# Optimization experiments

Measured on AMD Instinct MI355X. Metric: run time of the kernel, lower is better.

## Reference

```python
import math
import jax, jax.numpy as jnp
import numpy as np

# Gemma4Audio config constants
HID = 1024
H = 8
D = HID // H            # 128
CHUNK = 12              # attention_chunk_size
PAST = 13 - 1           # max_past_horizon = context_left - 1
FUT = 0                 # max_future_horizon = context_right
CTX = CHUNK + PAST + FUT  # 24
SOFTCAP = 50.0
Q_SCALE = D ** (-0.5) / math.log(2)
K_SCALE = math.log(1.0 + math.e) / math.log(2)


def setup_inputs() -> dict:
    key = jax.random.key(0)
    ks = jax.random.split(key, 8)
    B, S = 4, 6144
    P = CTX + 1  # 25 relative positions
    std = HID ** (-0.5)
    return {
        "hidden_states": jax.random.normal(ks[0], (B, S, HID), jnp.float32),
        "position_embeddings": jax.random.normal(ks[1], (P, HID), jnp.float32),
        "Wq": jax.random.normal(ks[2], (HID, HID), jnp.float32) * std,
        "Wk": jax.random.normal(ks[3], (HID, HID), jnp.float32) * std,
        "Wv": jax.random.normal(ks[4], (HID, HID), jnp.float32) * std,
        "Wpost": jax.random.normal(ks[5], (HID, HID), jnp.float32) * std,
        "Wrel": jax.random.normal(ks[6], (HID, HID), jnp.float32) * std,
        "per_dim_scale": jnp.zeros((D,), jnp.float32),  # torch init: zeros
    }


def _extract_block_context(x, num_blocks):
    # x: [B, S, H, D] -> [B, num_blocks, CTX, H, D]
    xp = jnp.pad(x, ((0, 0), (PAST, FUT + CHUNK - 1), (0, 0), (0, 0)))
    idx = jnp.arange(num_blocks)[:, None] * CHUNK + jnp.arange(CTX)[None, :]
    return xp[:, idx]  # gather along seq axis


def _rel_shift(x):
    # x: [B, H, nb, CHUNK, P] -> [B, H, nb, CHUNK, CTX]
    B, Hh, nb, bs, pos_len = x.shape
    x = jnp.pad(x, ((0, 0), (0, 0), (0, 0), (0, 0), (0, CTX + 1 - pos_len)))
    x = x.reshape(B, Hh, nb, bs * (CTX + 1))[..., : bs * CTX]
    return x.reshape(B, Hh, nb, bs, CTX)


def reference(hidden_states, position_embeddings, Wq, Wk, Wv, Wpost, Wrel, per_dim_scale):
    B, S, _ = hidden_states.shape
    nb = (S + CHUNK - 1) // CHUNK
    pad = nb * CHUNK - S

    # Projections (ClippableLinear clamps are +/-inf at init -> identity)
    q = (hidden_states @ Wq.T).reshape(B, S, H, D)
    k = (hidden_states @ Wk.T).reshape(B, S, H, D)
    v = (hidden_states @ Wv.T).reshape(B, S, H, D)

    q = q * (Q_SCALE * jax.nn.softplus(per_dim_scale))  # per-dim scaled queries
    k = k * K_SCALE

    # [B, nb, CHUNK, H, D]
    q_blocked = jnp.pad(q, ((0, 0), (0, pad), (0, 0), (0, 0))).reshape(B, nb, CHUNK, H, D)
    k_ctx = _extract_block_context(k, nb)  # [B, nb, CTX, H, D]
    v_ctx = _extract_block_context(v, nb)

    # content score: [B, H, nb, CHUNK, CTX]
    matrix_ac = jnp.einsum('bnchd,bnkhd->bhnck', q_blocked, k_ctx)

    # relative position score
    rel_k = (position_embeddings @ Wrel.T).reshape(-1, H, D)  # [P, H, D]
    matrix_bd = jnp.einsum('bnchd,phd->bhncp', q_blocked, rel_k)
    matrix_bd = _rel_shift(matrix_bd)  # [B, H, nb, CHUNK, CTX]

    logits = matrix_ac + matrix_bd
    logits = jnp.tanh(logits / SOFTCAP) * SOFTCAP  # softcap
    attn = jax.nn.softmax(logits, axis=-1)

    out = jnp.einsum('bhnck,bnkhd->bnchd', attn, v_ctx)
    out = out.reshape(B, nb * CHUNK, H * D)[:, :S]
    return out @ Wpost.T
```

## Files before the change

### kernel.cpp

```cpp
#include <hip/hip_runtime.h>
#include <hip/hip_bf16.h>
#include <math.h>

typedef unsigned short ushort_t;
typedef __attribute__((ext_vector_type(8))) short short8;
typedef __attribute__((ext_vector_type(4))) short s4v;
typedef __attribute__((ext_vector_type(4))) float float4v;

#define HID 1024
#define NH 8
#define DH 128
#define CHUNK 12
#define PAST 12
#define CTX 24
#define NPOS 25
#define QKVW 3072

__device__ __forceinline__ float bf2f(ushort_t b){
  union{unsigned int u; float f;} x; x.u = ((unsigned int)b)<<16; return x.f;
}
__device__ __forceinline__ ushort_t f2bf(float f){
  union{float f; unsigned int u;} x; x.f = f;
  unsigned int u = x.u;
  unsigned int r = u + 0x7fffu + ((u>>16)&1u);
  return (ushort_t)(r>>16);
}

__device__ __forceinline__ void gload16(const ushort_t* g, ushort_t* l){
  __builtin_amdgcn_global_load_lds(
      (const __attribute__((address_space(1))) unsigned int*)g,
      (__attribute__((address_space(3))) unsigned int*)l,
      16, 0, 0);
}

__global__ __launch_bounds__(256) void cvt_f2b(
    const float* __restrict__ in, ushort_t* __restrict__ out, int n4)
{
  for (int i = blockIdx.x*256 + threadIdx.x; i < n4; i += gridDim.x*256){
    float4v v = ((const float4v*)in)[i];
    s4v o;
#pragma unroll
    for (int j=0;j<4;j++) o[j] = (short)f2bf(v[j]);
    ((s4v*)out)[i] = o;
  }
}

__global__ __launch_bounds__(256) void cvt_w4(
    const float* __restrict__ Wq, const float* __restrict__ Wk,
    const float* __restrict__ Wv, const float* __restrict__ Wp,
    ushort_t* __restrict__ Wcat, ushort_t* __restrict__ Wpb, int wsz4)
{
  for (int i = blockIdx.x*256 + threadIdx.x; i < 4*wsz4; i += gridDim.x*256){
    int seg = i / wsz4, off = i - seg*wsz4;
    const float* src = (seg==0) ? Wq : (seg==1) ? Wk : (seg==2) ? Wv : Wp;
    float4v v = ((const float4v*)src)[off];
    s4v o;
#pragma unroll
    for (int j=0;j<4;j++) o[j] = (short)f2bf(v[j]);
    if (seg < 3) ((s4v*)Wcat)[seg*wsz4 + off] = o;
    else         ((s4v*)Wpb)[off] = o;
  }
}

template<int MODE, int OUTF>
__global__ __launch_bounds__(256) void gemm3(
    const ushort_t* __restrict__ A, const ushort_t* __restrict__ W,
    void* __restrict__ Cv, int M, int N, int K,
    const float* __restrict__ pds, float qsc, float ksc)
{
  const int nwg  = gridDim.x;
  const int orig = blockIdx.x;
  const int qch  = nwg >> 3, rch = nwg & 7;
  const int xcd  = orig & 7, idx = orig >> 3;
  const int bid  = (xcd < rch ? xcd*(qch+1) : rch*(qch+1) + (xcd-rch)*qch) + idx;

  const int NT = N >> 7;
  const int m0 = (bid / NT) * 128;
  const int n0 = (bid % NT) * 128;

  const int tid  = threadIdx.x;
  const int w    = tid >> 6, lane = tid & 63;
  const int wm   = w >> 1, wn = w & 1;
  const int lr   = lane & 15;
  const int lg   = lane >> 4;

  __shared__ ushort_t slab[6*128*32];
  ushort_t* a0 = slab;                 ushort_t* b0 = slab + 128*32;
  ushort_t* a1 = slab + 2*128*32;      ushort_t* b1 = slab + 3*128*32;
  ushort_t* a2 = slab + 4*128*32;      ushort_t* b2 = slab + 5*128*32;

  float4v acc[4][4];
#pragma unroll
  for (int i=0;i<4;i++)
#pragma unroll
    for (int j=0;j<4;j++) acc[i][j] = (float4v)0.0f;

  const int sr = lane >> 2;
  const int sc = (lane & 3) * 8;

  const ushort_t* Ab0 = A + (size_t)(m0 + w*16      + sr)*K + sc;
  const ushort_t* Ab1 = A + (size_t)(m0 + 64 + w*16 + sr)*K + sc;
  const ushort_t* Bb0 = W + (size_t)(n0 + w*16      + sr)*K + sc;
  const ushort_t* Bb1 = W + (size_t)(n0 + 64 + w*16 + sr)*K + sc;

#define STAGE(Abuf, Bbuf, kt) do {                    \
    gload16(Ab0 + (kt), &(Abuf)[(w*16)*32]);          \
    gload16(Ab1 + (kt), &(Abuf)[(64 + w*16)*32]);     \
    gload16(Bb0 + (kt), &(Bbuf)[(w*16)*32]);          \
    gload16(Bb1 + (kt), &(Bbuf)[(64 + w*16)*32]);     \
  } while(0)

#define COMPUTE(Abuf, Bbuf) do {                                             \
    short8 afr[4], bfr[4];                                                   \
    _Pragma("unroll")                                                        \
    for (int i=0;i<4;i++) afr[i] = *(const short8*)&(Abuf)[(wm*64 + i*16 + lr)*32 + lg*8]; \
    _Pragma("unroll")                                                        \
    for (int j=0;j<4;j++) bfr[j] = *(const short8*)&(Bbuf)[(wn*64 + j*16 + lr)*32 + lg*8]; \
    __builtin_amdgcn_s_setprio(1);                                           \
    _Pragma("unroll")                                                        \
    for (int i=0;i<4;i++)                                                    \
      _Pragma("unroll")                                                      \
      for (int j=0;j<4;j++)                                                  \
        acc[i][j] = __builtin_amdgcn_mfma_f32_16x16x32_bf16(afr[i], bfr[j], acc[i][j], 0,0,0); \
    __builtin_amdgcn_s_setprio(0);                                           \
  } while(0)

  const int nt = K >> 5;
  STAGE(a0, b0, 0);
  STAGE(a1, b1, 32);

  for (int t = 0; t < nt; ++t){
    if (t == nt-1) asm volatile("s_waitcnt vmcnt(0)" ::: "memory");
    else           asm volatile("s_waitcnt vmcnt(4)" ::: "memory");
    asm volatile("s_barrier" ::: "memory");
    if (t+2 < nt) STAGE(a2, b2, (t+2)*32);
    COMPUTE(a0, b0);
    ushort_t* ta = a0; a0 = a1; a1 = a2; a2 = ta;
    ushort_t* tb = b0; b0 = b1; b1 = b2; b2 = tb;
  }
#undef STAGE
#undef COMPUTE

  __syncthreads();

  if (OUTF == 0){
#pragma unroll
    for (int j=0;j<4;j++){
      const int col = wn*64 + j*16 + lr;
      float scale = 1.0f;
      if (MODE==1){
        const int gcol = n0 + col;
        if (gcol < 1024){ float p = pds[gcol & (DH-1)]; scale = qsc * log1pf(expf(p)); }
        else if (gcol < 2048) scale = ksc;
      }
#pragma unroll
      for (int i=0;i<4;i++){
        const int row = wm*64 + i*16 + lg*4;
#pragma unroll
        for (int r=0;r<4;r++)
          slab[(row + r)*128 + col] = f2bf(acc[i][j][r] * scale);
      }
    }
    __syncthreads();
    ushort_t* Crow = (ushort_t*)Cv + (size_t)m0*N + n0;
    const int rr = tid >> 4, sl = (tid & 15)*8;
#pragma unroll
    for (int it=0; it<8; ++it){
      const int row = it*16 + rr;
      *(short8*)&Crow[(size_t)row*N + sl] = *(const short8*)&slab[row*128 + sl];
    }
  } else {
    float* smf = (float*)slab;
    float* Crow = (float*)Cv + (size_t)m0*N + n0;
#pragma unroll
    for (int h2=0; h2<2; ++h2){
      __syncthreads();
      if (wm == h2){
#pragma unroll
        for (int j=0;j<4;j++){
          const int col = wn*64 + j*16 + lr;
#pragma unroll
          for (int i=0;i<4;i++){
            const int row = i*16 + lg*4;
#pragma unroll
            for (int r=0;r<4;r++)
              smf[(row + r)*128 + col] = acc[i][j][r];
          }
        }
      }
      __syncthreads();
      const int rr = tid >> 5, half = ((tid >> 4) & 1)*64, sl = (tid & 15)*4;
#pragma unroll
      for (int it=0; it<8; ++it){
        const int row = it*8 + rr;
        *(float4v*)&Crow[(size_t)(h2*64 + row)*N + half + sl] =
            *(const float4v*)&smf[row*128 + half + sl];
      }
    }
  }
}

__global__ __launch_bounds__(256) void relk_kernel(
    const float* __restrict__ pe, const float* __restrict__ Wrel,
    ushort_t* __restrict__ rel)
{
  int gid = blockIdx.x*256 + threadIdx.x;
  if (gid >= NPOS*HID) return;
  int p = gid >> 10, n = gid & 1023;
  const float* a = pe + p*HID;
  const float* w = Wrel + (size_t)n*HID;
  float s = 0.f;
  for (int k=0;k<HID;k+=4){
    float4v av = *(const float4v*)(a+k);
    float4v wv = *(const float4v*)(w+k);
#pragma unroll
    for (int u=0;u<4;u++) s += av[u]*wv[u];
  }
  rel[gid] = f2bf(s);
}

__global__ __launch_bounds__(256) void attn_kernel(
  const ushort_t* __restrict__ qkv, const ushort_t* __restrict__ rel,
  ushort_t* __restrict__ o, int S)
{
  const int n0 = blockIdx.x * 4;
  const int b  = blockIdx.y, h = blockIdx.z;
  const int tid = threadIdx.x;
  const size_t bS = (size_t)b * S;

  __shared__ ushort_t ks[68][136];
  __shared__ ushort_t vt[128][68];
  __shared__ float    sA[4][12][36];
  __shared__ float    sB[4][12][36];
  __shared__ ushort_t Pp[4][16][40];

  const int base = n0*CHUNK - PAST;
  {
    const int r0 = tid >> 4;
    const int c0 = (tid & 15) * 8;
    for (int r = r0; r < 68; r += 16){
      int s = base + r;
      short8 kv = (short8)0, vv = (short8)0;
      if (r < 60 && s >= 0 && s < S){
        kv = *(const short8*)&qkv[(bS + s)*QKVW + 1024 + h*DH + c0];
        vv = *(const short8*)&qkv[(bS + s)*QKVW + 2048 + h*DH + c0];
      }
      *(short8*)&ks[r][c0] = kv;
#pragma unroll
      for (int u=0;u<8;u++) vt[c0+u][r] = (ushort_t)vv[u];
    }
  }
  __syncthreads();

  const int w    = tid >> 6;
  const int lane = tid & 63;
  const int lr   = lane & 15;
  const int lg   = lane >> 4;

  int qrow = (n0 + w)*CHUNK + lr;
  if (qrow >= S) qrow = S - 1;
  const ushort_t* qp = qkv + (bS + qrow)*QKVW + h*DH + lg*8;
  short8 qf[4];
#pragma unroll
  for (int ks2=0; ks2<4; ks2++) qf[ks2] = *(const short8*)(qp + ks2*32);

#pragma unroll
  for (int t0=0; t0<2; t0++){
    float4v acc = (float4v)0.0f;
#pragma unroll
    for (int ks2=0; ks2<4; ks2++){
      short8 kf = *(const short8*)&ks[w*CHUNK + t0*16 + lr][ks2*32 + lg*8];
      acc = __builtin_amdgcn_mfma_f32_16x16x32_bf16(qf[ks2], kf, acc, 0,0,0);
    }
#pragma unroll
    for (int reg=0; reg<4; reg++){
      int cr = lg*4 + reg;
      if (cr < CHUNK) sA[w][cr][t0*16 + lr] = acc[reg];
    }
  }

  const ushort_t* rp = rel + h*DH;
#pragma unroll
  for (int t0=0; t0<2; t0++){
    float4v acc = (float4v)0.0f;
#pragma unroll
    for (int ks2=0; ks2<4; ks2++){
      short8 rf = *(const short8*)(rp + (size_t)(t0*16 + lr)*HID + ks2*32 + lg*8);
      acc = __builtin_amdgcn_mfma_f32_16x16x32_bf16(qf[ks2], rf, acc, 0,0,0);
    }
#pragma unroll
    for (int reg=0; reg<4; reg++){
      int cr = lg*4 + reg;
      if (cr < CHUNK) sB[w][cr][t0*16 + lr] = acc[reg];
    }
  }

#pragma unroll
  for (int i=0;i<2;i++){
    int idx = i*64 + lane;
    *(s4v*)&Pp[w][idx>>3][(idx&7)*4] = (s4v)0;
  }

  {
    const int c2 = lane >> 5;
    const int t  = lane & 31;
#pragma unroll
    for (int i=0;i<6;i++){
      int c = i*2 + c2;
      float x = -1e30f;
      if (t < CTX){
        int f = c*CTX + t;
        int r = f / NPOS, p = f - r*NPOS;
        x = sA[w][c][t] + sB[w][r][p];
        x = 50.0f * tanhf(x * 0.02f);
      }
      float m = x;
      for (int off=16; off>=1; off>>=1) m = fmaxf(m, __shfl_xor(m, off, 32));
      float e = (t < CTX) ? expf(x - m) : 0.0f;
      float s = e;
      for (int off=16; off>=1; off>>=1) s += __shfl_xor(s, off, 32);
      if (t < CTX) Pp[w][c][t] = f2bf(e / s);
    }
  }

  short8 pf = *(const short8*)&Pp[w][lr][lg*8];
  const int orow_base = (n0 + w)*CHUNK;
#pragma unroll
  for (int j=0; j<8; j++){
    int d  = j*16 + lr;
    int tb = w*CHUNK + lg*8;
    s4v b0 = *(const s4v*)&vt[d][tb];
    s4v b1 = *(const s4v*)&vt[d][tb+4];
    short8 bf;
#pragma unroll
    for (int u=0;u<4;u++){ bf[u] = b0[u]; bf[u+4] = b1[u]; }
    float4v a = __builtin_amdgcn_mfma_f32_16x16x32_bf16(pf, bf, (float4v)0.0f, 0,0,0);
#pragma unroll
    for (int reg=0; reg<4; reg++){
      int cr = lg*4 + reg;
      if (cr < CHUNK)
        o[(bS + orow_base + cr)*HID + h*DH + j*16 + lr] = f2bf(a[reg]);
    }
  }
}

extern "C" void kernel_launch(void* const* d_in, const int* in_sizes, int n_in,
                              void* d_out, int out_size, void* d_ws, size_t ws_size,
                              hipStream_t stream)
{
  const float* hs    = (const float*)d_in[0];
  const float* pe    = (const float*)d_in[1];
  const float* Wq    = (const float*)d_in[2];
  const float* Wk    = (const float*)d_in[3];
  const float* Wv    = (const float*)d_in[4];
  const float* Wpost = (const float*)d_in[5];
  const float* Wrel  = (const float*)d_in[6];
  const float* pds   = (const float*)d_in[7];
  float* out = (float*)d_out;

  const int BS = in_sizes[0] / HID;
  const int B  = 4;
  const int S  = BS / B;
  const int nb = S / CHUNK;

  const size_t per = (size_t)BS * HID;
  const size_t wsz = (size_t)HID * HID;
  ushort_t* qkv  = (ushort_t*)d_ws;
  ushort_t* at   = qkv  + (size_t)BS * QKVW;
  ushort_t* rel  = at   + per;
  ushort_t* hsb  = rel  + (size_t)NPOS*HID;
  ushort_t* Wcat = hsb  + per;
  ushort_t* Wpb  = Wcat + 3*wsz;

  const float qsc = (float)(pow((double)DH, -0.5) / log(2.0));
  const float ksc = (float)(log(1.0 + exp(1.0)) / log(2.0));

  cvt_f2b<<<2048, 256, 0, stream>>>(hs, hsb, (int)(per/4));
  cvt_w4<<<2048, 256, 0, stream>>>(Wq, Wk, Wv, Wpost, Wcat, Wpb, (int)(wsz/4));

  gemm3<1,0><<<(BS/128)*(QKVW/128), 256, 0, stream>>>(
      hsb, Wcat, qkv, BS, QKVW, HID, pds, qsc, ksc);
  relk_kernel<<<(NPOS*HID + 255)/256, 256, 0, stream>>>(pe, Wrel, rel);
  attn_kernel<<<dim3(nb/4, B, NH), 256, 0, stream>>>(qkv, rel, at, S);
  gemm3<0,1><<<(BS/128)*(HID/128), 256, 0, stream>>>(
      at, Wpb, out, BS, HID, HID, nullptr, 1.0f, 1.0f);
}
```

Baseline: 427.8 us.

## Merge conversion kernels, split relk dot across lane pairs, shrink attention LDS

Merges the two fp32-to-bf16 conversion kernels into one launch and moves the rel-key projection ahead of the QKV GEMM. The rel-key kernel now splits each 1024-long dot product across two lanes and combines them with a shuffle. The attention kernel stages the rel keys in LDS and packs all its scratch arrays into one aliased shared buffer, reusing regions across phases behind extra barriers. The aim is fewer launches, more parallelism in the rel-key projection, lower LDS use for better occupancy, and fewer scattered global loads, at the cost of two more __syncthreads in attention.

```diff
diff --git a/kernel.cpp b/kernel.cpp
--- a/kernel.cpp
+++ b/kernel.cpp
@@ -33,32 +33,27 @@
       16, 0, 0);
 }
 
-__global__ __launch_bounds__(256) void cvt_f2b(
-    const float* __restrict__ in, ushort_t* __restrict__ out, int n4)
-{
-  for (int i = blockIdx.x*256 + threadIdx.x; i < n4; i += gridDim.x*256){
-    float4v v = ((const float4v*)in)[i];
+__global__ __launch_bounds__(256) void cvt_all(
+    const float* __restrict__ hs, const float* __restrict__ Wq,
+    const float* __restrict__ Wk, const float* __restrict__ Wv,
+    const float* __restrict__ Wp, ushort_t* __restrict__ hsb,
+    ushort_t* __restrict__ Wcat, ushort_t* __restrict__ Wpb, int nhs4)
+{
+  const int W4 = 262144;
+  const int total = nhs4 + 4*W4;
+  for (int i = blockIdx.x*256 + threadIdx.x; i < total; i += gridDim.x*256){
+    const float4v* src; s4v* dst; int off;
+    if (i < nhs4){ src = (const float4v*)hs; dst = (s4v*)hsb; off = i; }
+    else {
+      int j = i - nhs4; int seg = j >> 18; off = j & (W4-1);
+      src = (const float4v*)(seg==0?Wq:seg==1?Wk:seg==2?Wv:Wp);
+      dst = (seg<3) ? ((s4v*)Wcat) + (size_t)seg*W4 : (s4v*)Wpb;
+    }
+    float4v v = src[off];
     s4v o;
 #pragma unroll
-    for (int j=0;j<4;j++) o[j] = (short)f2bf(v[j]);
-    ((s4v*)out)[i] = o;
-  }
-}
-
-__global__ __launch_bounds__(256) void cvt_w4(
-    const float* __restrict__ Wq, const float* __restrict__ Wk,
-    const float* __restrict__ Wv, const float* __restrict__ Wp,
-    ushort_t* __restrict__ Wcat, ushort_t* __restrict__ Wpb, int wsz4)
-{
-  for (int i = blockIdx.x*256 + threadIdx.x; i < 4*wsz4; i += gridDim.x*256){
-    int seg = i / wsz4, off = i - seg*wsz4;
-    const float* src = (seg==0) ? Wq : (seg==1) ? Wk : (seg==2) ? Wv : Wp;
-    float4v v = ((const float4v*)src)[off];
-    s4v o;
-#pragma unroll
-    for (int j=0;j<4;j++) o[j] = (short)f2bf(v[j]);
-    if (seg < 3) ((s4v*)Wcat)[seg*wsz4 + off] = o;
-    else         ((s4v*)Wpb)[off] = o;
+    for (int j2=0;j2<4;j2++) o[j2] = (short)f2bf(v[j2]);
+    dst[off] = o;
   }
 }
 
@@ -200,23 +195,25 @@
   }
 }
 
-__global__ __launch_bounds__(256) void relk_kernel(
+__global__ __launch_bounds__(256) void relk2(
     const float* __restrict__ pe, const float* __restrict__ Wrel,
     ushort_t* __restrict__ rel)
 {
-  int gid = blockIdx.x*256 + threadIdx.x;
-  if (gid >= NPOS*HID) return;
-  int p = gid >> 10, n = gid & 1023;
-  const float* a = pe + p*HID;
-  const float* w = Wrel + (size_t)n*HID;
+  int g = blockIdx.x*256 + threadIdx.x;
+  int idx = g >> 1, par = g & 1;
+  if (idx >= NPOS*HID) return;
+  int p = idx >> 10, n = idx & 1023;
+  const float* a = pe + p*HID + par*512;
+  const float* w = Wrel + (size_t)n*HID + par*512;
   float s = 0.f;
-  for (int k=0;k<HID;k+=4){
+  for (int k=0;k<512;k+=4){
     float4v av = *(const float4v*)(a+k);
     float4v wv = *(const float4v*)(w+k);
 #pragma unroll
     for (int u=0;u<4;u++) s += av[u]*wv[u];
   }
-  rel[gid] = f2bf(s);
+  s += __shfl_xor(s, 1, 64);
+  if (!par) rel[idx] = f2bf(s);
 }
 
 __global__ __launch_bounds__(256) void attn_kernel(
@@ -228,11 +225,12 @@
   const int tid = threadIdx.x;
   const size_t bS = (size_t)b * S;
 
-  __shared__ ushort_t ks[68][136];
-  __shared__ ushort_t vt[128][68];
-  __shared__ float    sA[4][12][36];
-  __shared__ float    sB[4][12][36];
-  __shared__ ushort_t Pp[4][16][40];
+  __shared__ ushort_t lds[24800];
+  ushort_t* ks = lds;
+  ushort_t* vt = lds + 9248;
+  float*    sB = (float*)(lds + 17952);
+  ushort_t* rs = lds + 20448;
+  float*    sA = (float*)(lds + 20448);
 
   const int base = n0*CHUNK - PAST;
   {
@@ -245,9 +243,14 @@
         kv = *(const short8*)&qkv[(bS + s)*QKVW + 1024 + h*DH + c0];
         vv = *(const short8*)&qkv[(bS + s)*QKVW + 2048 + h*DH + c0];
       }
-      *(short8*)&ks[r][c0] = kv;
-#pragma unroll
-      for (int u=0;u<8;u++) vt[c0+u][r] = (ushort_t)vv[u];
+      *(short8*)&ks[r*136 + c0] = kv;
+#pragma unroll
+      for (int u=0;u<8;u++) vt[(c0+u)*68 + r] = (ushort_t)vv[u];
+    }
+    for (int r = r0; r < 32; r += 16){
+      short8 rv = (short8)0;
+      if (r < NPOS) rv = *(const short8*)&rel[r*HID + h*DH + c0];
+      *(short8*)&rs[r*136 + c0] = rv;
     }
   }
   __syncthreads();
@@ -257,6 +260,10 @@
   const int lr   = lane & 15;
   const int lg   = lane >> 4;
 
+  float*    sAw = sA + w*312;
+  float*    sBw = sB + w*312;
+  ushort_t* Ppw = lds + w*640;
+
   int qrow = (n0 + w)*CHUNK + lr;
   if (qrow >= S) qrow = S - 1;
   const ushort_t* qp = qkv + (bS + qrow)*QKVW + h*DH + lg*8;
@@ -269,37 +276,36 @@
     float4v acc = (float4v)0.0f;
 #pragma unroll
     for (int ks2=0; ks2<4; ks2++){
-      short8 kf = *(const short8*)&ks[w*CHUNK + t0*16 + lr][ks2*32 + lg*8];
-      acc = __builtin_amdgcn_mfma_f32_16x16x32_bf16(qf[ks2], kf, acc, 0,0,0);
-    }
+      short8 rf = *(const short8*)&rs[(t0*16 + lr)*136 + ks2*32 + lg*8];
+      acc = __builtin_amdgcn_mfma_f32_16x16x32_bf16(qf[ks2], rf, acc, 0,0,0);
+    }
+    const int p = t0*16 + lr;
 #pragma unroll
     for (int reg=0; reg<4; reg++){
       int cr = lg*4 + reg;
-      if (cr < CHUNK) sA[w][cr][t0*16 + lr] = acc[reg];
-    }
-  }
-
-  const ushort_t* rp = rel + h*DH;
+      if (cr < CHUNK && p < NPOS) sBw[cr*26 + p] = acc[reg];
+    }
+  }
+  __syncthreads();
+
 #pragma unroll
   for (int t0=0; t0<2; t0++){
     float4v acc = (float4v)0.0f;
 #pragma unroll
     for (int ks2=0; ks2<4; ks2++){
-      short8 rf = *(const short8*)(rp + (size_t)(t0*16 + lr)*HID + ks2*32 + lg*8);
-      acc = __builtin_amdgcn_mfma_f32_16x16x32_bf16(qf[ks2], rf, acc, 0,0,0);
-    }
+      short8 kf = *(const short8*)&ks[(w*CHUNK + t0*16 + lr)*136 + ks2*32 + lg*8];
+      acc = __builtin_amdgcn_mfma_f32_16x16x32_bf16(qf[ks2], kf, acc, 0,0,0);
+    }
+    const int t = t0*16 + lr;
 #pragma unroll
     for (int reg=0; reg<4; reg++){
       int cr = lg*4 + reg;
-      if (cr < CHUNK) sB[w][cr][t0*16 + lr] = acc[reg];
-    }
-  }
-
-#pragma unroll
-  for (int i=0;i<2;i++){
-    int idx = i*64 + lane;
-    *(s4v*)&Pp[w][idx>>3][(idx&7)*4] = (s4v)0;
-  }
+      if (cr < CHUNK && t < CTX) sAw[cr*26 + t] = acc[reg];
+    }
+  }
+  __syncthreads();
+
+  if (lane < CHUNK) *(short8*)&Ppw[lane*40 + 24] = (short8)0;
 
   {
     const int c2 = lane >> 5;
@@ -311,7 +317,7 @@
       if (t < CTX){
         int f = c*CTX + t;
         int r = f / NPOS, p = f - r*NPOS;
-        x = sA[w][c][t] + sB[w][r][p];
+        x = sAw[c*26 + t] + sBw[r*26 + p];
         x = 50.0f * tanhf(x * 0.02f);
       }
       float m = x;
@@ -319,18 +325,18 @@
       float e = (t < CTX) ? expf(x - m) : 0.0f;
       float s = e;
       for (int off=16; off>=1; off>>=1) s += __shfl_xor(s, off, 32);
-      if (t < CTX) Pp[w][c][t] = f2bf(e / s);
-    }
-  }
-
-  short8 pf = *(const short8*)&Pp[w][lr][lg*8];
+      if (t < CTX) Ppw[c*40 + t] = f2bf(e / s);
+    }
+  }
+
+  short8 pf = *(const short8*)&Ppw[lr*40 + lg*8];
   const int orow_base = (n0 + w)*CHUNK;
 #pragma unroll
   for (int j=0; j<8; j++){
     int d  = j*16 + lr;
     int tb = w*CHUNK + lg*8;
-    s4v b0 = *(const s4v*)&vt[d][tb];
-    s4v b1 = *(const s4v*)&vt[d][tb+4];
+    s4v b0 = *(const s4v*)&vt[d*68 + tb];
+    s4v b1 = *(const s4v*)&vt[d*68 + tb + 4];
     short8 bf;
 #pragma unroll
     for (int u=0;u<4;u++){ bf[u] = b0[u]; bf[u+4] = b1[u]; }
@@ -375,12 +381,12 @@
   const float qsc = (float)(pow((double)DH, -0.5) / log(2.0));
   const float ksc = (float)(log(1.0 + exp(1.0)) / log(2.0));
 
-  cvt_f2b<<<2048, 256, 0, stream>>>(hs, hsb, (int)(per/4));
-  cvt_w4<<<2048, 256, 0, stream>>>(Wq, Wk, Wv, Wpost, Wcat, Wpb, (int)(wsz/4));
+  cvt_all<<<4096, 256, 0, stream>>>(hs, Wq, Wk, Wv, Wpost, hsb, Wcat, Wpb,
+                                    (int)(per/4));
+  relk2<<<200, 256, 0, stream>>>(pe, Wrel, rel);
 
   gemm3<1,0><<<(BS/128)*(QKVW/128), 256, 0, stream>>>(
       hsb, Wcat, qkv, BS, QKVW, HID, pds, qsc, ksc);
-  relk_kernel<<<(NPOS*HID + 255)/256, 256, 0, stream>>>(pe, Wrel, rel);
   attn_kernel<<<dim3(nb/4, B, NH), 256, 0, stream>>>(qkv, rel, at, S);
   gemm3<0,1><<<(BS/128)*(HID/128), 256, 0, stream>>>(
       at, Wpb, out, BS, HID, HID, nullptr, 1.0f, 1.0f);
```

Result: faster. 386.6 us (-9.6%).
